# Kernel optimization log

Measured on AMD Instinct MI355X. Metric: run time of the kernel, lower is better.

The kernel has to match this reference:

```python
import jax, jax.numpy as jnp
import numpy as np

C_M, C_Z, C = 256, 128, 32
N_SEQ, N_RES = 128, 256


def setup_inputs() -> dict:
    key = jax.random.key(0)
    ks = jax.random.split(key, 8)
    m = jax.random.normal(ks[0], (N_SEQ, N_RES, C_M), dtype=jnp.float32)
    gamma = jnp.ones((C_M,), dtype=jnp.float32)
    beta = jnp.zeros((C_M,), dtype=jnp.float32)
    s = 1.0 / np.sqrt(C_M)
    W1 = jax.random.normal(ks[1], (C_M, C), dtype=jnp.float32) * s
    b1 = jax.random.normal(ks[2], (C,), dtype=jnp.float32) * 0.01
    W2 = jax.random.normal(ks[3], (C_M, C), dtype=jnp.float32) * s
    b2 = jax.random.normal(ks[4], (C,), dtype=jnp.float32) * 0.01
    Wout = jax.random.normal(ks[5], (C * C, C_Z), dtype=jnp.float32) / np.sqrt(C * C)
    bout = jax.random.normal(ks[6], (C_Z,), dtype=jnp.float32) * 0.01
    return {"m": m, "gamma": gamma, "beta": beta, "W1": W1, "b1": b1,
            "W2": W2, "b2": b2, "Wout": Wout, "bout": bout}


def _layernorm(x, gamma, beta, eps=1e-5):
    mu = jnp.mean(x, axis=-1, keepdims=True)
    var = jnp.var(x, axis=-1, keepdims=True)
    return (x - mu) * jax.lax.rsqrt(var + eps) * gamma + beta


def reference(m, gamma, beta, W1, b1, W2, b2, Wout, bout):
    n_seq = m.shape[-3]
    mn = _layernorm(m, gamma, beta)              # (s, i, c_m)
    a = mn @ W1 + b1                              # (s, i, c)
    b = mn @ W2 + b2                              # (s, j, c)
    o = jnp.einsum('sic,sjk->ijck', a, b)        # (i, j, c, c)
    o = o.reshape(o.shape[0], o.shape[1], -1)    # (i, j, c*c)
    z = (o @ Wout + bout) / n_seq                # (i, j, c_z)
    return z
```

## Files before the change

### kernel.cpp

```cpp
#include <hip/hip_runtime.h>
#include <hip/hip_bf16.h>

typedef __attribute__((ext_vector_type(8))) short short8;
typedef __attribute__((ext_vector_type(4))) short short4v;
typedef __attribute__((ext_vector_type(4))) float f32x4;

#define WS_A   0
#define WS_B   (8192 * 128 * 2)
#define WS_WT  (2 * 8192 * 128 * 2)
#define WS_W12 (WS_WT + 128 * 1024 * 2)

static __device__ __forceinline__ short f2bf(float x) {
    __hip_bfloat16 h = __float2bfloat16(x);
    return *reinterpret_cast<short*>(&h);
}

typedef __attribute__((address_space(3))) unsigned int lds_u32;
typedef const __attribute__((address_space(1))) unsigned int glb_u32;
static __device__ __forceinline__ void stage16(const void* g, void* l) {
    __builtin_amdgcn_global_load_lds((glb_u32*)g, (lds_u32*)l, 16, 0, 0);
}

__global__ __launch_bounds__(256) void k_prep(const float* __restrict__ Wout,
                                              const float* __restrict__ W1,
                                              const float* __restrict__ W2,
                                              __hip_bfloat16* __restrict__ WoutT,
                                              __hip_bfloat16* __restrict__ W12bf) {
    int idx = blockIdx.x * 256 + threadIdx.x;
    if (blockIdx.x < 512) {
        int z = idx >> 10, ck = idx & 1023;
        WoutT[idx] = __float2bfloat16(Wout[ck * 128 + z]);
    } else {
        idx -= 512 * 256;
        int c = idx >> 8, d = idx & 255;
        W12bf[idx] = __float2bfloat16(c < 32 ? W1[d * 32 + c] : W2[d * 32 + (c - 32)]);
    }
}

__global__ __launch_bounds__(256) void k_lnproj(const float* __restrict__ mm,
                                                const float* __restrict__ gamma,
                                                const float* __restrict__ beta,
                                                const float* __restrict__ b1,
                                                const float* __restrict__ b2,
                                                const __hip_bfloat16* __restrict__ W12bf,
                                                __hip_bfloat16* __restrict__ Ap,
                                                __hip_bfloat16* __restrict__ Bp) {
    __shared__ char sMN[4][8192];
    const int lane = threadIdx.x & 63;
    const int wid  = threadIdx.x >> 6;
    const int gw   = blockIdx.x * 4 + wid;
    const int i_   = gw & 255;
    const int sb   = (gw >> 8) * 16;

    float4 g4  = *(const float4*)&gamma[lane * 4];
    float4 be4 = *(const float4*)&beta[lane * 4];
    char* my = sMN[wid];

    #pragma unroll
    for (int rr = 0; rr < 16; rr++) {
        float4 x = *(const float4*)&mm[((size_t)(sb + rr) * 256 + i_) * 256 + lane * 4];
        float s  = x.x + x.y + x.z + x.w;
        float ss = x.x * x.x + x.y * x.y + x.z * x.z + x.w * x.w;
        #pragma unroll
        for (int off = 32; off; off >>= 1) {
            s  += __shfl_xor(s, off);
            ss += __shfl_xor(ss, off);
        }
        float mu  = s * (1.f / 256.f);
        float var = ss * (1.f / 256.f) - mu * mu;
        float rs  = rsqrtf(var + 1e-5f);
        short4v v;
        v.x = f2bf((x.x - mu) * rs * g4.x + be4.x);
        v.y = f2bf((x.y - mu) * rs * g4.y + be4.y);
        v.z = f2bf((x.z - mu) * rs * g4.z + be4.z);
        v.w = f2bf((x.w - mu) * rs * g4.w + be4.w);
        *(short4v*)(my + rr * 512 + ((lane * 8) ^ ((rr & 7) << 4))) = v;
    }

    const short* wt12 = (const short*)W12bf;
    const int g = lane >> 4, r16 = lane & 15;

    f32x4 acc[4];
    #pragma unroll
    for (int nf = 0; nf < 4; nf++) {
        int col = nf * 16 + r16;
        float bv = (col < 32) ? b1[col] : b2[col - 32];
        acc[nf] = (f32x4){bv, bv, bv, bv};
    }
    #pragma unroll
    for (int ks = 0; ks < 8; ks++) {
        int L = ks * 64 + g * 16;
        short8 af = *(const short8*)(my + r16 * 512 + (L ^ ((r16 & 7) << 4)));
        #pragma unroll
        for (int nf = 0; nf < 4; nf++) {
            short8 bfv = *(const short8*)&wt12[(nf * 16 + r16) * 256 + ks * 32 + g * 8];
            acc[nf] = __builtin_amdgcn_mfma_f32_16x16x32_bf16(af, bfv, acc[nf], 0, 0, 0);
        }
    }
    #pragma unroll
    for (int nf = 0; nf < 4; nf++) {
        int col = nf * 16 + r16;
        short* Out = (short*)((col < 32) ? Ap : Bp);
        int cr = col & 31;
        short4v v;
        v.x = f2bf(acc[nf][0]); v.y = f2bf(acc[nf][1]);
        v.z = f2bf(acc[nf][2]); v.w = f2bf(acc[nf][3]);
        *(short4v*)&Out[(i_ * 32 + cr) * 128 + sb + g * 4] = v;
    }
}

extern __shared__ char lds[];

__global__ __launch_bounds__(512, 2) void k_gemm4(const __hip_bfloat16* __restrict__ Apb,
                                                  const __hip_bfloat16* __restrict__ Bpb,
                                                  const __hip_bfloat16* __restrict__ WoutT,
                                                  const float* __restrict__ bout,
                                                  float* __restrict__ out) {
    const int t = threadIdx.x, lane = t & 63, wid = t >> 6;
    const int g = lane >> 4, r16 = lane & 15;
    const int wr = wid >> 2, wc = wid & 3;
    const int bi = blockIdx.x >> 5, bj = blockIdx.x & 31;

    const short* gA = (const short*)Apb + (size_t)bi * 256 * 128;
    const short* gB = (const short*)Bpb + (size_t)bj * 256 * 128;

    const int srow8 = lane >> 3;
    const int sgran = (lane & 7) ^ srow8;
    #pragma unroll
    for (int kh = 0; kh < 2; kh++) {
        #pragma unroll
        for (int rd = 0; rd < 4; rd++) {
            const int row = rd * 64 + wid * 8 + srow8;
            stage16(gB + row * 128 + kh * 64 + sgran * 8,
                    lds + kh * 65536 + rd * 8192 + wid * 1024);
            stage16(gA + row * 128 + kh * 64 + sgran * 8,
                    lds + kh * 65536 + 32768 + rd * 8192 + wid * 1024);
        }
    }

    asm volatile("s_waitcnt vmcnt(8)" ::: "memory");
    __builtin_amdgcn_s_barrier();

    f32x4 acc[8][4];
    #pragma unroll
    for (int mf = 0; mf < 8; mf++)
        #pragma unroll
        for (int nf = 0; nf < 4; nf++)
            acc[mf][nf] = (f32x4){0.f, 0.f, 0.f, 0.f};

    #pragma unroll
    for (int kh = 0; kh < 2; kh++) {
        if (kh) {
            asm volatile("s_waitcnt vmcnt(0)" ::: "memory");
            __builtin_amdgcn_s_barrier();
        }
        const char* sBb = lds + kh * 65536;
        const char* sAb = lds + kh * 65536 + 32768;
        #pragma unroll
        for (int ksl = 0; ksl < 2; ksl++) {
            short8 af[8], bfv[4];
            #pragma unroll
            for (int mf = 0; mf < 8; mf++) {
                const int row = wr * 128 + mf * 16 + r16;
                af[mf] = *(const short8*)(sBb + row * 128 + (((ksl * 4 + g) ^ (row & 7)) << 4));
            }
            #pragma unroll
            for (int nf = 0; nf < 4; nf++) {
                const int row = wc * 64 + nf * 16 + r16;
                bfv[nf] = *(const short8*)(sAb + row * 128 + (((ksl * 4 + g) ^ (row & 7)) << 4));
            }
            __builtin_amdgcn_s_setprio(1);
            #pragma unroll
            for (int mf = 0; mf < 8; mf++)
                #pragma unroll
                for (int nf = 0; nf < 4; nf++)
                    acc[mf][nf] = __builtin_amdgcn_mfma_f32_16x16x32_bf16(af[mf], bfv[nf], acc[mf][nf], 0, 0, 0);
            __builtin_amdgcn_s_setprio(0);
        }
    }
    __builtin_amdgcn_s_barrier();

    const int z = wid * 16 + r16;
    const float bv = bout[z];
    f32x4 acc2[4];
    #pragma unroll
    for (int pf = 0; pf < 4; pf++) acc2[pf] = (f32x4){bv, bv, bv, bv};
    const short* wt = (const short*)WoutT;

    #define REPACK(h)                                                                    \
        {                                                                                \
            char* sPh = lds + (h) * 65536;                                               \
            _Pragma("unroll")                                                            \
            for (int nq = 0; nq < 2; nq++) {                                             \
                const int nf = (h) + nq * 2;                                             \
                const int p = (wc * 2 + nq) * 8 + wr * 4;                                \
                _Pragma("unroll")                                                        \
                for (int mf = 0; mf < 8; mf++) {                                         \
                    const int pp = p + (mf >> 1);                                        \
                    const int L = r16 * 64 + (mf & 1) * 32 + g * 8;                      \
                    short4v v;                                                           \
                    v.x = f2bf(acc[mf][nf][0]); v.y = f2bf(acc[mf][nf][1]);              \
                    v.z = f2bf(acc[mf][nf][2]); v.w = f2bf(acc[mf][nf][3]);              \
                    *(short4v*)(sPh + pp * 1024 + (L ^ ((((L >> 7) ^ pp) & 7) << 4))) = v; \
                }                                                                        \
            }                                                                            \
        }

    #define EPI(h)                                                                       \
        {                                                                                \
            const char* sPh = lds + (h) * 65536;                                         \
            _Pragma("unroll 4")                                                          \
            for (int ks = 0; ks < 16; ks++) {                                            \
                short8 wf = *(const short8*)&wt[z * 1024 + (h) * 512 + ks * 32 + g * 8]; \
                _Pragma("unroll")                                                        \
                for (int pf = 0; pf < 4; pf++) {                                         \
                    const int row = pf * 16 + r16;                                       \
                    const int L = ks * 64 + g * 16;                                      \
                    short8 pv = *(const short8*)(sPh + row * 1024 +                      \
                                                 (L ^ ((((L >> 7) ^ row) & 7) << 4)));   \
                    acc2[pf] = __builtin_amdgcn_mfma_f32_16x16x32_bf16(pv, wf, acc2[pf], 0, 0, 0); \
                }                                                                        \
            }                                                                            \
        }

    REPACK(0)
    asm volatile("s_waitcnt lgkmcnt(0)" ::: "memory");
    __builtin_amdgcn_s_barrier();
    REPACK(1)
    EPI(0)
    asm volatile("s_waitcnt lgkmcnt(0)" ::: "memory");
    __builtin_amdgcn_s_barrier();
    EPI(1)

    #pragma unroll
    for (int pf = 0; pf < 4; pf++) {
        #pragma unroll
        for (int reg = 0; reg < 4; reg++) {
            const int p = pf * 16 + g * 4 + reg;
            const int ig = bi * 8 + (p >> 3), jg = bj * 8 + (p & 7);
            out[((size_t)(ig * 256 + jg)) * 128 + z] = acc2[pf][reg] * (1.f / 128.f);
        }
    }
    #undef REPACK
    #undef EPI
}

extern "C" void kernel_launch(void* const* d_in, const int* in_sizes, int n_in,
                              void* d_out, int out_size, void* d_ws, size_t ws_size,
                              hipStream_t stream) {
    const float* mm    = (const float*)d_in[0];
    const float* gamma = (const float*)d_in[1];
    const float* beta  = (const float*)d_in[2];
    const float* W1    = (const float*)d_in[3];
    const float* b1    = (const float*)d_in[4];
    const float* W2    = (const float*)d_in[5];
    const float* b2    = (const float*)d_in[6];
    const float* Wout  = (const float*)d_in[7];
    const float* bout  = (const float*)d_in[8];

    __hip_bfloat16* Ap    = (__hip_bfloat16*)((char*)d_ws + WS_A);
    __hip_bfloat16* Bp    = (__hip_bfloat16*)((char*)d_ws + WS_B);
    __hip_bfloat16* WoutT = (__hip_bfloat16*)((char*)d_ws + WS_WT);
    __hip_bfloat16* W12bf = (__hip_bfloat16*)((char*)d_ws + WS_W12);
    float* out = (float*)d_out;

    (void)hipFuncSetAttribute(reinterpret_cast<const void*>(k_gemm4),
                              hipFuncAttributeMaxDynamicSharedMemorySize, 131072);

    hipLaunchKernelGGL(k_prep, dim3(576), dim3(256), 0, stream, Wout, W1, W2, WoutT, W12bf);
    hipLaunchKernelGGL(k_lnproj, dim3(512), dim3(256), 0, stream,
                       mm, gamma, beta, b1, b2, W12bf, Ap, Bp);
    hipLaunchKernelGGL(k_gemm4, dim3(1024), dim3(512), 131072, stream,
                       Ap, Bp, WoutT, bout, out);
}
```

Measured before the change: 76.97 us.

## Stage W12 in LDS, remap gemm blocks, double-buffer Wout loads in epilogue

k_lnproj now copies the bf16 W1/W2 weights into swizzled LDS once per block and reads its MFMA B-fragments from there instead of global memory. In the main GEMM kernel, block IDs are remapped so that consecutive blocks spread across bi/bj, which changes L2/XCD locality. The Wout epilogue is restructured into double-buffered register prefetch groups (WLOAD/WCOMP) with raised priority during MFMAs, so global weight loads overlap with compute. Launch bounds change from 2 to 1 block per CU, which allows more registers but is a hint that may reduce occupancy.

```diff
diff --git a/kernel.cpp b/kernel.cpp
--- a/kernel.cpp
+++ b/kernel.cpp
@@ -46,11 +46,22 @@
                                                 __hip_bfloat16* __restrict__ Ap,
                                                 __hip_bfloat16* __restrict__ Bp) {
     __shared__ char sMN[4][8192];
-    const int lane = threadIdx.x & 63;
-    const int wid  = threadIdx.x >> 6;
+    __shared__ char sW[32768];
+    const int t    = threadIdx.x;
+    const int lane = t & 63;
+    const int wid  = t >> 6;
     const int gw   = blockIdx.x * 4 + wid;
     const int i_   = gw & 255;
     const int sb   = (gw >> 8) * 16;
+
+    #pragma unroll
+    for (int it = 0; it < 8; it++) {
+        const int idx = it * 256 + t;
+        const int row = idx >> 5;
+        const int L   = (idx & 31) * 16;
+        *(short8*)(sW + row * 512 + (L ^ ((row & 7) << 4))) =
+            *(const short8*)((const short*)W12bf + idx * 8);
+    }
 
     float4 g4  = *(const float4*)&gamma[lane * 4];
     float4 be4 = *(const float4*)&beta[lane * 4];
@@ -76,8 +87,8 @@
         v.w = f2bf((x.w - mu) * rs * g4.w + be4.w);
         *(short4v*)(my + rr * 512 + ((lane * 8) ^ ((rr & 7) << 4))) = v;
     }
-
-    const short* wt12 = (const short*)W12bf;
+    __syncthreads();
+
     const int g = lane >> 4, r16 = lane & 15;
 
     f32x4 acc[4];
@@ -89,11 +100,11 @@
     }
     #pragma unroll
     for (int ks = 0; ks < 8; ks++) {
-        int L = ks * 64 + g * 16;
+        const int L = ks * 64 + g * 16;
         short8 af = *(const short8*)(my + r16 * 512 + (L ^ ((r16 & 7) << 4)));
         #pragma unroll
         for (int nf = 0; nf < 4; nf++) {
-            short8 bfv = *(const short8*)&wt12[(nf * 16 + r16) * 256 + ks * 32 + g * 8];
+            short8 bfv = *(const short8*)(sW + (nf * 16 + r16) * 512 + (L ^ ((r16 & 7) << 4)));
             acc[nf] = __builtin_amdgcn_mfma_f32_16x16x32_bf16(af, bfv, acc[nf], 0, 0, 0);
         }
     }
@@ -111,7 +122,7 @@
 
 extern __shared__ char lds[];
 
-__global__ __launch_bounds__(512, 2) void k_gemm4(const __hip_bfloat16* __restrict__ Apb,
+__global__ __launch_bounds__(512, 1) void k_gemm6(const __hip_bfloat16* __restrict__ Apb,
                                                   const __hip_bfloat16* __restrict__ Bpb,
                                                   const __hip_bfloat16* __restrict__ WoutT,
                                                   const float* __restrict__ bout,
@@ -119,7 +130,8 @@
     const int t = threadIdx.x, lane = t & 63, wid = t >> 6;
     const int g = lane >> 4, r16 = lane & 15;
     const int wr = wid >> 2, wc = wid & 3;
-    const int bi = blockIdx.x >> 5, bj = blockIdx.x & 31;
+    const int bid = (blockIdx.x & 7) * 128 + (blockIdx.x >> 3);
+    const int bi = bid >> 5, bj = bid & 31;
 
     const short* gA = (const short*)Apb + (size_t)bi * 256 * 128;
     const short* gB = (const short*)Bpb + (size_t)bj * 256 * 128;
@@ -185,7 +197,34 @@
     f32x4 acc2[4];
     #pragma unroll
     for (int pf = 0; pf < 4; pf++) acc2[pf] = (f32x4){bv, bv, bv, bv};
-    const short* wt = (const short*)WoutT;
+    const short* wtz = (const short*)WoutT + z * 1024 + g * 8;
+
+    short8 wA[4], wB[4];
+
+    #define WLOAD(buf, h, grp)                                                           \
+        {                                                                                \
+            _Pragma("unroll")                                                            \
+            for (int q = 0; q < 4; q++)                                                  \
+                buf[q] = *(const short8*)&wtz[(h) * 512 + ((grp) * 4 + q) * 32];         \
+        }
+
+    #define WCOMP(buf, h, grp)                                                           \
+        {                                                                                \
+            const char* sPh = lds + (h) * 65536;                                         \
+            __builtin_amdgcn_s_setprio(1);                                               \
+            _Pragma("unroll")                                                            \
+            for (int q = 0; q < 4; q++) {                                                \
+                const int L = ((grp) * 4 + q) * 64 + g * 16;                             \
+                _Pragma("unroll")                                                        \
+                for (int pf = 0; pf < 4; pf++) {                                         \
+                    const int row = pf * 16 + r16;                                       \
+                    short8 pv = *(const short8*)(sPh + row * 1024 +                      \
+                                                 (L ^ ((((L >> 7) ^ row) & 7) << 4)));   \
+                    acc2[pf] = __builtin_amdgcn_mfma_f32_16x16x32_bf16(pv, buf[q], acc2[pf], 0, 0, 0); \
+                }                                                                        \
+            }                                                                            \
+            __builtin_amdgcn_s_setprio(0);                                               \
+        }
 
     #define REPACK(h)                                                                    \
         {                                                                                \
@@ -206,31 +245,25 @@
             }                                                                            \
         }
 
-    #define EPI(h)                                                                       \
-        {                                                                                \
-            const char* sPh = lds + (h) * 65536;                                         \
-            _Pragma("unroll 4")                                                          \
-            for (int ks = 0; ks < 16; ks++) {                                            \
-                short8 wf = *(const short8*)&wt[z * 1024 + (h) * 512 + ks * 32 + g * 8]; \
-                _Pragma("unroll")                                                        \
-                for (int pf = 0; pf < 4; pf++) {                                         \
-                    const int row = pf * 16 + r16;                                       \
-                    const int L = ks * 64 + g * 16;                                      \
-                    short8 pv = *(const short8*)(sPh + row * 1024 +                      \
-                                                 (L ^ ((((L >> 7) ^ row) & 7) << 4)));   \
-                    acc2[pf] = __builtin_amdgcn_mfma_f32_16x16x32_bf16(pv, wf, acc2[pf], 0, 0, 0); \
-                }                                                                        \
-            }                                                                            \
-        }
-
+    WLOAD(wA, 0, 0)
+    WLOAD(wB, 0, 1)
     REPACK(0)
     asm volatile("s_waitcnt lgkmcnt(0)" ::: "memory");
     __builtin_amdgcn_s_barrier();
     REPACK(1)
-    EPI(0)
+
+    WCOMP(wA, 0, 0) WLOAD(wA, 0, 2)
+    WCOMP(wB, 0, 1) WLOAD(wB, 0, 3)
+    WCOMP(wA, 0, 2) WLOAD(wA, 1, 0)
+    WCOMP(wB, 0, 3) WLOAD(wB, 1, 1)
+
     asm volatile("s_waitcnt lgkmcnt(0)" ::: "memory");
     __builtin_amdgcn_s_barrier();
-    EPI(1)
+
+    WCOMP(wA, 1, 0) WLOAD(wA, 1, 2)
+    WCOMP(wB, 1, 1) WLOAD(wB, 1, 3)
+    WCOMP(wA, 1, 2)
+    WCOMP(wB, 1, 3)
 
     #pragma unroll
     for (int pf = 0; pf < 4; pf++) {
@@ -242,7 +275,8 @@
         }
     }
     #undef REPACK
-    #undef EPI
+    #undef WLOAD
+    #undef WCOMP
 }
 
 extern "C" void kernel_launch(void* const* d_in, const int* in_sizes, int n_in,
@@ -264,12 +298,12 @@
     __hip_bfloat16* W12bf = (__hip_bfloat16*)((char*)d_ws + WS_W12);
     float* out = (float*)d_out;
 
-    (void)hipFuncSetAttribute(reinterpret_cast<const void*>(k_gemm4),
+    (void)hipFuncSetAttribute(reinterpret_cast<const void*>(k_gemm6),
                               hipFuncAttributeMaxDynamicSharedMemorySize, 131072);
 
     hipLaunchKernelGGL(k_prep, dim3(576), dim3(256), 0, stream, Wout, W1, W2, WoutT, W12bf);
     hipLaunchKernelGGL(k_lnproj, dim3(512), dim3(256), 0, stream,
                        mm, gamma, beta, b1, b2, W12bf, Ap, Bp);
-    hipLaunchKernelGGL(k_gemm4, dim3(1024), dim3(512), 131072, stream,
+    hipLaunchKernelGGL(k_gemm6, dim3(1024), dim3(512), 131072, stream,
                        Ap, Bp, WoutT, bout, out);
 }
```

Result: faster. 71.51 us (-7.1%).
